# Optimization experiments

Hardware: AMD Instinct MI355X
Metric: run time of the kernel (lower is better)

## Reference

```python
import jax, jax.numpy as jnp
import numpy as np

B, IN, HID, GH, K, A = 131072, 256, 128, 64, 4, 3
EPS = 1e-5

def _ln(x, g, b):
    mu = jnp.mean(x, axis=-1, keepdims=True)
    var = jnp.mean((x - mu) ** 2, axis=-1, keepdims=True)
    return (x - mu) * jax.lax.rsqrt(var + EPS) * g + b

def _expert(x, blend, W, bias):
    # math-equivalent to einsum('bk,koi->boi') + bmm: blend after per-expert matvec
    per_exp = jnp.einsum('bi,koi->bko', x, W)          # [B,K,out]
    return jnp.einsum('bk,bko->bo', blend, per_exp) + blend @ bias

def setup_inputs() -> dict:
    key = jax.random.key(0)
    ks = jax.random.split(key, 8)
    d = {}
    d['state'] = jax.random.normal(ks[0], (B, IN), jnp.float32)
    # gating network
    d['gw1'] = jax.random.normal(ks[1], (GH, IN), jnp.float32) / np.sqrt(IN)
    d['gb1'] = jnp.zeros((GH,), jnp.float32)
    d['gln_g'] = jnp.ones((GH,), jnp.float32)
    d['gln_b'] = jnp.zeros((GH,), jnp.float32)
    d['gw2'] = jax.random.normal(ks[2], (K, GH), jnp.float32) / np.sqrt(GH)
    d['gb2'] = jnp.zeros((K,), jnp.float32)
    d['temperature'] = jnp.ones((1,), jnp.float32)
    # experts: weight [K, out, in] with kaiming-like init sqrt(2/in)
    d['e1_w'] = jax.random.normal(ks[3], (K, HID, IN), jnp.float32) * np.sqrt(2.0 / IN)
    d['e1_b'] = jnp.zeros((K, HID), jnp.float32)
    d['ln1_g'] = jnp.ones((HID,), jnp.float32)
    d['ln1_b'] = jnp.zeros((HID,), jnp.float32)
    d['e2_w'] = jax.random.normal(ks[4], (K, HID, HID), jnp.float32) * np.sqrt(2.0 / HID)
    d['e2_b'] = jnp.zeros((K, HID), jnp.float32)
    d['ln2_g'] = jnp.ones((HID,), jnp.float32)
    d['ln2_b'] = jnp.zeros((HID,), jnp.float32)
    d['e3_w'] = jax.random.normal(ks[5], (K, A, HID), jnp.float32) * np.sqrt(2.0 / HID)
    d['e3_b'] = jnp.zeros((K, A), jnp.float32)
    return d

def reference(state, gw1, gb1, gln_g, gln_b, gw2, gb2, temperature,
              e1_w, e1_b, ln1_g, ln1_b, e2_w, e2_b, ln2_g, ln2_b, e3_w, e3_b):
    # gating
    h = jax.nn.relu(_ln(state @ gw1.T + gb1, gln_g, gln_b))
    logits = h @ gw2.T + gb2
    temp = jnp.clip(temperature, 0.1, 2.0)
    blend = jax.nn.softmax(logits / temp, axis=-1)       # [B,K]
    # expert stack
    x = jax.nn.relu(_ln(_expert(state, blend, e1_w, e1_b), ln1_g, ln1_b))
    x = jax.nn.relu(_ln(_expert(x, blend, e2_w, e2_b), ln2_g, ln2_b))
    policy_logits = _expert(x, blend, e3_w, e3_b)        # [B,A]
    return policy_logits, blend
```

## Files before the change

kernel.cpp:

```cpp
#include <hip/hip_runtime.h>


typedef __attribute__((ext_vector_type(8))) short short8;
typedef __attribute__((ext_vector_type(4))) float f32x4;

constexpr int B_TOT = 131072;
constexpr int IN    = 256;
constexpr int HID   = 128;
constexpr int GH    = 64;
constexpr int NA    = 3;
constexpr int ROWS  = 64;
constexpr int XS    = 264;
constexpr int BS    = 132;
constexpr float EPS = 1e-5f;

constexpr int O_G1H = 0;
constexpr int O_E1H = 32768;
constexpr int O_E2H = 294912;

__device__ __forceinline__ unsigned short bf16h(float f) {
  unsigned int u = __float_as_uint(f);
  return (unsigned short)((u + 0x7FFFu + ((u >> 16) & 1u)) >> 16);
}
__device__ __forceinline__ float bf16f(unsigned short h) {
  return __uint_as_float(((unsigned int)h) << 16);
}

__global__ __launch_bounds__(256) void prep_w(
    const float* __restrict__ gw1, const float* __restrict__ e1w,
    const float* __restrict__ e2w, unsigned short* __restrict__ ws)
{
  const int NT = 16384 + 131072 + 65536;
  for (int d = blockIdx.x * 256 + threadIdx.x; d < NT; d += gridDim.x * 256) {
    float v; int dst, lo_off;
    if (d < 16384) {
      int d2 = d; int j = d2 & 7, lane = (d2 >> 3) & 63, kc = (d2 >> 9) & 7, gt = d2 >> 12;
      int o = gt * 16 + (lane & 15), k = kc * 32 + (lane >> 4) * 8 + j;
      v = gw1[o * IN + k]; dst = O_G1H + d2; lo_off = 16384;
    } else if (d < 147456) {
      int d2 = d - 16384; int j = d2 & 7, lane = (d2 >> 3) & 63, kc = (d2 >> 9) & 7,
          ot = (d2 >> 12) & 7, ke = d2 >> 15;
      int o = ot * 16 + (lane & 15), k = kc * 32 + (lane >> 4) * 8 + j;
      v = e1w[ke * HID * IN + o * IN + k]; dst = O_E1H + d2; lo_off = 131072;
    } else {
      int d2 = d - 147456; int j = d2 & 7, lane = (d2 >> 3) & 63, kc = (d2 >> 9) & 3,
          ot = (d2 >> 11) & 7, ke = d2 >> 14;
      int o = ot * 16 + (lane & 15), k = kc * 32 + (lane >> 4) * 8 + j;
      v = e2w[ke * HID * HID + o * HID + k]; dst = O_E2H + d2; lo_off = 65536;
    }
    unsigned short h = bf16h(v);
    ws[dst] = h;
    ws[dst + lo_off] = bf16h(v - bf16f(h));
  }
}

#define MFMA(a, b, c) __builtin_amdgcn_mfma_f32_16x16x32_bf16((a), (b), (c), 0, 0, 0)

__global__ __launch_bounds__(512) void mann_mfma(
    const float* __restrict__ state,
    const float* __restrict__ gb1,
    const float* __restrict__ gln_g, const float* __restrict__ gln_b,
    const float* __restrict__ gw2, const float* __restrict__ gb2,
    const float* __restrict__ temperature,
    const float* __restrict__ e1_b,
    const float* __restrict__ ln1_g, const float* __restrict__ ln1_b,
    const float* __restrict__ e2_b,
    const float* __restrict__ ln2_g, const float* __restrict__ ln2_b,
    const float* __restrict__ e3_w, const float* __restrict__ e3_b,
    const unsigned short* __restrict__ wf,
    float* __restrict__ out_policy, float* __restrict__ out_blend)
{
  __shared__ __align__(16) unsigned char smem[75264];
  unsigned short* xh = (unsigned short*)smem;
  unsigned short* xl = (unsigned short*)(smem + 33792);
  unsigned short* ah = (unsigned short*)smem;
  unsigned short* al = (unsigned short*)(smem + 16384);
  float* bt    = (float*)(smem + 33792);
  float* ps    = (float*)(smem + 67584);
  float* stats = (float*)(smem + 69632);
  float* lp    = (float*)(smem + 70144);
  float* sbl   = (float*)(smem + 74240);

  const int tid = threadIdx.x;
  const int lane = tid & 63, wv = tid >> 6;
  const int l15 = lane & 15, l4 = lane >> 4;
  const int rh = wv >> 2, oq = wv & 3;
  const int rowbase = blockIdx.x * ROWS;
  const f32x4 zz = {0.f, 0.f, 0.f, 0.f};

  {
    const float4* gsrc = (const float4*)(state + (size_t)rowbase * IN);
#pragma unroll
    for (int it = 0; it < 8; ++it) {
      int fi = tid + it * 512;
      int row = fi >> 6, c4 = fi & 63;
      float4 v = gsrc[fi];
      int base = row * XS + c4 * 4;
      float vv[4] = {v.x, v.y, v.z, v.w};
#pragma unroll
      for (int e = 0; e < 4; ++e) {
        unsigned short h = bf16h(vv[e]);
        xh[base + e] = h;
        xl[base + e] = bf16h(vv[e] - bf16f(h));
      }
    }
  }
  __syncthreads();

  {
    f32x4 g[2] = {zz, zz};
    const unsigned short* wpg = wf + O_G1H + (oq * 8 * 64 + (size_t)lane) * 8;
#pragma unroll 1
    for (int kc = 0; kc < 8; ++kc) {
      short8 wh = *(const short8*)(wpg + kc * 512);
      short8 wl = *(const short8*)(wpg + kc * 512 + 16384);
#pragma unroll
      for (int rt = 0; rt < 2; ++rt) {
        int row = rh * 32 + rt * 16 + l15;
        int xo = row * XS + kc * 32 + l4 * 8;
        short8 xhf = *(const short8*)&xh[xo];
        short8 xlf = *(const short8*)&xl[xo];
        g[rt] = MFMA(xhf, wh, g[rt]);
        g[rt] = MFMA(xlf, wh, g[rt]);
        g[rt] = MFMA(xhf, wl, g[rt]);
      }
    }
    const float bv = gb1[oq * 16 + l15];
#pragma unroll
    for (int rt = 0; rt < 2; ++rt)
#pragma unroll
      for (int r = 0; r < 4; ++r) {
        g[rt][r] += bv;
        float sv = g[rt][r], qv = g[rt][r] * g[rt][r];
#pragma unroll
        for (int m = 1; m < 16; m <<= 1) { sv += __shfl_xor(sv, m, 64); qv += __shfl_xor(qv, m, 64); }
        if (l15 == 0) {
          int row = rh * 32 + rt * 16 + l4 * 4 + r;
          ps[(row * 4 + oq) * 2 + 0] = sv;
          ps[(row * 4 + oq) * 2 + 1] = qv;
        }
      }
    __syncthreads();
    if (tid < 64) {
      float s = 0.f, q = 0.f;
#pragma unroll
      for (int o = 0; o < 4; ++o) { s += ps[(tid * 4 + o) * 2]; q += ps[(tid * 4 + o) * 2 + 1]; }
      float mu = s * (1.f / GH), var = q * (1.f / GH) - mu * mu;
      stats[tid * 2] = mu; stats[tid * 2 + 1] = rsqrtf(var + EPS);
    }
    __syncthreads();
    const float gg = gln_g[oq * 16 + l15], gbb = gln_b[oq * 16 + l15];
    float g2[4];
#pragma unroll
    for (int k = 0; k < 4; ++k) g2[k] = gw2[k * GH + oq * 16 + l15];
#pragma unroll
    for (int rt = 0; rt < 2; ++rt)
#pragma unroll
      for (int r = 0; r < 4; ++r) {
        int row = rh * 32 + rt * 16 + l4 * 4 + r;
        float mu = stats[row * 2], rstd = stats[row * 2 + 1];
        float h = fmaxf((g[rt][r] - mu) * rstd * gg + gbb, 0.f);
#pragma unroll
        for (int k = 0; k < 4; ++k) {
          float pv = h * g2[k];
#pragma unroll
          for (int m = 1; m < 16; m <<= 1) pv += __shfl_xor(pv, m, 64);
          if (l15 == 0) lp[(row * 4 + oq) * 4 + k] = pv;
        }
      }
  }
  __syncthreads();

  if (tid < 256) {
    int row = tid >> 2, kk = tid & 3;
    float lg = lp[(row * 4 + 0) * 4 + kk] + lp[(row * 4 + 1) * 4 + kk] +
               lp[(row * 4 + 2) * 4 + kk] + lp[(row * 4 + 3) * 4 + kk] + gb2[kk];
    float t = fminf(fmaxf(temperature[0], 0.1f), 2.0f);
    lg /= t;
    float mx = lg;
    mx = fmaxf(mx, __shfl_xor(mx, 1, 64));
    mx = fmaxf(mx, __shfl_xor(mx, 2, 64));
    float e = expf(lg - mx);
    float su = e;
    su += __shfl_xor(su, 1, 64);
    su += __shfl_xor(su, 2, 64);
    float bl = e / su;
    sbl[row * 4 + kk] = bl;
    out_blend[(size_t)(rowbase + row) * 4 + kk] = bl;
  }
  __syncthreads();

  f32x4 accb[2][2] = {{zz, zz}, {zz, zz}};

#pragma unroll
  for (int ke = 0; ke < 4; ++ke) {
    f32x4 t[2][2] = {{zz, zz}, {zz, zz}};
    const unsigned short* wp1 = wf + O_E1H + (((ke * 8 + oq * 2) * 8) * 64 + (size_t)lane) * 8;
#pragma unroll 1
    for (int kc = 0; kc < 8; ++kc) {
      short8 xhf[2], xlf[2];
#pragma unroll
      for (int rt = 0; rt < 2; ++rt) {
        int row = rh * 32 + rt * 16 + l15;
        int xo = row * XS + kc * 32 + l4 * 8;
        xhf[rt] = *(const short8*)&xh[xo];
        xlf[rt] = *(const short8*)&xl[xo];
      }
#pragma unroll
      for (int ot = 0; ot < 2; ++ot) {
        const unsigned short* p = wp1 + ot * 4096 + kc * 512;
        short8 wh = *(const short8*)p;
        short8 wl = *(const short8*)(p + 131072);
#pragma unroll
        for (int rt = 0; rt < 2; ++rt) {
          t[rt][ot] = MFMA(xhf[rt], wh, t[rt][ot]);
          t[rt][ot] = MFMA(xlf[rt], wh, t[rt][ot]);
          t[rt][ot] = MFMA(xhf[rt], wl, t[rt][ot]);
        }
      }
    }
    const float bv0 = e1_b[ke * HID + oq * 32 + l15];
    const float bv1 = e1_b[ke * HID + oq * 32 + 16 + l15];
#pragma unroll
    for (int rt = 0; rt < 2; ++rt)
#pragma unroll
      for (int r = 0; r < 4; ++r) {
        int row = rh * 32 + rt * 16 + l4 * 4 + r;
        float blv = sbl[row * 4 + ke];
        accb[rt][0][r] += blv * (t[rt][0][r] + bv0);
        accb[rt][1][r] += blv * (t[rt][1][r] + bv1);
      }
  }
#pragma unroll
  for (int rt = 0; rt < 2; ++rt)
#pragma unroll
    for (int r = 0; r < 4; ++r) {
      float sv = accb[rt][0][r] + accb[rt][1][r];
      float qv = accb[rt][0][r] * accb[rt][0][r] + accb[rt][1][r] * accb[rt][1][r];
#pragma unroll
      for (int m = 1; m < 16; m <<= 1) { sv += __shfl_xor(sv, m, 64); qv += __shfl_xor(qv, m, 64); }
      if (l15 == 0) {
        int row = rh * 32 + rt * 16 + l4 * 4 + r;
        ps[(row * 4 + oq) * 2 + 0] = sv;
        ps[(row * 4 + oq) * 2 + 1] = qv;
      }
    }
  __syncthreads();
  if (tid < 64) {
    float s = 0.f, q = 0.f;
#pragma unroll
    for (int o = 0; o < 4; ++o) { s += ps[(tid * 4 + o) * 2]; q += ps[(tid * 4 + o) * 2 + 1]; }
    float mu = s * (1.f / HID), var = q * (1.f / HID) - mu * mu;
    stats[tid * 2] = mu; stats[tid * 2 + 1] = rsqrtf(var + EPS);
  }
  __syncthreads();
  {
#pragma unroll
    for (int ot = 0; ot < 2; ++ot) {
      int c = oq * 32 + ot * 16 + l15;
      float lgv = ln1_g[c], lbv = ln1_b[c];
#pragma unroll
      for (int rt = 0; rt < 2; ++rt)
#pragma unroll
        for (int r = 0; r < 4; ++r) {
          int row = rh * 32 + rt * 16 + l4 * 4 + r;
          float mu = stats[row * 2], rstd = stats[row * 2 + 1];
          float y = fmaxf((accb[rt][ot][r] - mu) * rstd * lgv + lbv, 0.f);
          unsigned short h = bf16h(y);
          int idx = row * HID + (((c >> 3) ^ (row & 7)) << 3) + (c & 7);
          ah[idx] = h; al[idx] = bf16h(y - bf16f(h));
        }
    }
  }
  __syncthreads();

#pragma unroll
  for (int rt = 0; rt < 2; ++rt)
#pragma unroll
    for (int ot = 0; ot < 2; ++ot) accb[rt][ot] = zz;
#pragma unroll
  for (int ke = 0; ke < 4; ++ke) {
    f32x4 t[2][2] = {{zz, zz}, {zz, zz}};
    const unsigned short* wp2 = wf + O_E2H + (((ke * 8 + oq * 2) * 4) * 64 + (size_t)lane) * 8;
#pragma unroll 1
    for (int kc = 0; kc < 4; ++kc) {
      short8 xhf[2], xlf[2];
#pragma unroll
      for (int rt = 0; rt < 2; ++rt) {
        int row = rh * 32 + rt * 16 + l15;
        int gidx = (kc * 4 + l4) ^ (row & 7);
        int idx = row * HID + gidx * 8;
        xhf[rt] = *(const short8*)&ah[idx];
        xlf[rt] = *(const short8*)&al[idx];
      }
#pragma unroll
      for (int ot = 0; ot < 2; ++ot) {
        const unsigned short* p = wp2 + ot * 2048 + kc * 512;
        short8 wh = *(const short8*)p;
        short8 wl = *(const short8*)(p + 65536);
#pragma unroll
        for (int rt = 0; rt < 2; ++rt) {
          t[rt][ot] = MFMA(xhf[rt], wh, t[rt][ot]);
          t[rt][ot] = MFMA(xlf[rt], wh, t[rt][ot]);
          t[rt][ot] = MFMA(xhf[rt], wl, t[rt][ot]);
        }
      }
    }
    const float bv0 = e2_b[ke * HID + oq * 32 + l15];
    const float bv1 = e2_b[ke * HID + oq * 32 + 16 + l15];
#pragma unroll
    for (int rt = 0; rt < 2; ++rt)
#pragma unroll
      for (int r = 0; r < 4; ++r) {
        int row = rh * 32 + rt * 16 + l4 * 4 + r;
        float blv = sbl[row * 4 + ke];
        accb[rt][0][r] += blv * (t[rt][0][r] + bv0);
        accb[rt][1][r] += blv * (t[rt][1][r] + bv1);
      }
  }
#pragma unroll
  for (int rt = 0; rt < 2; ++rt)
#pragma unroll
    for (int r = 0; r < 4; ++r) {
      float sv = accb[rt][0][r] + accb[rt][1][r];
      float qv = accb[rt][0][r] * accb[rt][0][r] + accb[rt][1][r] * accb[rt][1][r];
#pragma unroll
      for (int m = 1; m < 16; m <<= 1) { sv += __shfl_xor(sv, m, 64); qv += __shfl_xor(qv, m, 64); }
      if (l15 == 0) {
        int row = rh * 32 + rt * 16 + l4 * 4 + r;
        ps[(row * 4 + oq) * 2 + 0] = sv;
        ps[(row * 4 + oq) * 2 + 1] = qv;
      }
    }
  __syncthreads();
  if (tid < 64) {
    float s = 0.f, q = 0.f;
#pragma unroll
    for (int o = 0; o < 4; ++o) { s += ps[(tid * 4 + o) * 2]; q += ps[(tid * 4 + o) * 2 + 1]; }
    float mu = s * (1.f / HID), var = q * (1.f / HID) - mu * mu;
    stats[tid * 2] = mu; stats[tid * 2 + 1] = rsqrtf(var + EPS);
  }
  __syncthreads();
  {
#pragma unroll
    for (int ot = 0; ot < 2; ++ot) {
      int c = oq * 32 + ot * 16 + l15;
      float lgv = ln2_g[c], lbv = ln2_b[c];
#pragma unroll
      for (int rt = 0; rt < 2; ++rt)
#pragma unroll
        for (int r = 0; r < 4; ++r) {
          int row = rh * 32 + rt * 16 + l4 * 4 + r;
          float mu = stats[row * 2], rstd = stats[row * 2 + 1];
          float y = fmaxf((accb[rt][ot][r] - mu) * rstd * lgv + lbv, 0.f);
          bt[row * BS + c] = y;
        }
    }
  }
  __syncthreads();

  if (tid < 256) {
    int row = tid >> 2, kk = tid & 3;
    float p[NA] = {0.f, 0.f, 0.f};
#pragma unroll
    for (int ic = 0; ic < HID / 4; ++ic) {
      float4 xv = *(const float4*)&bt[row * BS + ic * 4];
#pragma unroll
      for (int a = 0; a < NA; ++a) {
        float4 wv = *(const float4*)&e3_w[(size_t)(kk * NA + a) * HID + ic * 4];
        p[a] = fmaf(xv.x, wv.x, fmaf(xv.y, wv.y, fmaf(xv.z, wv.z, fmaf(xv.w, wv.w, p[a]))));
      }
    }
    float blk = sbl[row * 4 + kk];
#pragma unroll
    for (int a = 0; a < NA; ++a) p[a] = blk * (p[a] + e3_b[kk * NA + a]);
#pragma unroll
    for (int a = 0; a < NA; ++a) {
      p[a] += __shfl_xor(p[a], 1, 64);
      p[a] += __shfl_xor(p[a], 2, 64);
    }
    if (kk == 0) {
      size_t o = (size_t)(rowbase + row) * NA;
      out_policy[o + 0] = p[0];
      out_policy[o + 1] = p[1];
      out_policy[o + 2] = p[2];
    }
  }
}

extern "C" void kernel_launch(void* const* d_in, const int* in_sizes, int n_in,
                              void* d_out, int out_size, void* d_ws, size_t ws_size,
                              hipStream_t stream) {
  const float* state = (const float*)d_in[0];
  const float* gw1   = (const float*)d_in[1];
  const float* gb1   = (const float*)d_in[2];
  const float* gln_g = (const float*)d_in[3];
  const float* gln_b = (const float*)d_in[4];
  const float* gw2   = (const float*)d_in[5];
  const float* gb2   = (const float*)d_in[6];
  const float* temp  = (const float*)d_in[7];
  const float* e1_w  = (const float*)d_in[8];
  const float* e1_b  = (const float*)d_in[9];
  const float* ln1_g = (const float*)d_in[10];
  const float* ln1_b = (const float*)d_in[11];
  const float* e2_w  = (const float*)d_in[12];
  const float* e2_b  = (const float*)d_in[13];
  const float* ln2_g = (const float*)d_in[14];
  const float* ln2_b = (const float*)d_in[15];
  const float* e3_w  = (const float*)d_in[16];
  const float* e3_b  = (const float*)d_in[17];

  unsigned short* wf = (unsigned short*)d_ws;
  float* out_policy = (float*)d_out;
  float* out_blend  = (float*)d_out + (size_t)B_TOT * NA;

  prep_w<<<832, 256, 0, stream>>>(gw1, e1_w, e2_w, wf);
  mann_mfma<<<B_TOT / ROWS, 512, 0, stream>>>(
      state, gb1, gln_g, gln_b, gw2, gb2, temp,
      e1_b, ln1_g, ln1_b, e2_b, ln2_g, ln2_b, e3_w, e3_b,
      wf, out_policy, out_blend);
}
```

Before: 600.4 us.

## Shrink row tile to 48, remap waves to output columns, swizzle LDS, atomic LN stats

Reduces the rows per block from 64 to 48 and gives each of the 8 waves a 16-column output slice over all 48 rows, where before waves were split by row half and column quarter. The padded LDS layouts are replaced with XOR-swizzled layouts, and the per-row LayerNorm partial sums are combined with LDS atomics instead of a partial-sum buffer. Together these cut shared memory to about 50KB and add a launch bound that asks for more resident waves, to improve occupancy and latency hiding. In exchange each wave reloads the activation tile for three row tiles, the grid gets a ragged tail with bounds checks, and the atomics change the floating-point summation order.

```diff
diff --git a/kernel.cpp b/kernel.cpp
--- a/kernel.cpp
+++ b/kernel.cpp
@@ -7,16 +7,9 @@
 constexpr int B_TOT = 131072;
 constexpr int IN    = 256;
 constexpr int HID   = 128;
-constexpr int GH    = 64;
 constexpr int NA    = 3;
-constexpr int ROWS  = 64;
-constexpr int XS    = 264;
-constexpr int BS    = 132;
+constexpr int ROWS  = 48;
 constexpr float EPS = 1e-5f;
-
-constexpr int O_G1H = 0;
-constexpr int O_E1H = 32768;
-constexpr int O_E2H = 294912;
 
 __device__ __forceinline__ unsigned short bf16h(float f) {
   unsigned int u = __float_as_uint(f);
@@ -36,17 +29,17 @@
     if (d < 16384) {
       int d2 = d; int j = d2 & 7, lane = (d2 >> 3) & 63, kc = (d2 >> 9) & 7, gt = d2 >> 12;
       int o = gt * 16 + (lane & 15), k = kc * 32 + (lane >> 4) * 8 + j;
-      v = gw1[o * IN + k]; dst = O_G1H + d2; lo_off = 16384;
+      v = gw1[o * IN + k]; dst = d2; lo_off = 16384;
     } else if (d < 147456) {
       int d2 = d - 16384; int j = d2 & 7, lane = (d2 >> 3) & 63, kc = (d2 >> 9) & 7,
           ot = (d2 >> 12) & 7, ke = d2 >> 15;
       int o = ot * 16 + (lane & 15), k = kc * 32 + (lane >> 4) * 8 + j;
-      v = e1w[ke * HID * IN + o * IN + k]; dst = O_E1H + d2; lo_off = 131072;
+      v = e1w[ke * HID * IN + o * IN + k]; dst = 32768 + d2; lo_off = 131072;
     } else {
       int d2 = d - 147456; int j = d2 & 7, lane = (d2 >> 3) & 63, kc = (d2 >> 9) & 3,
           ot = (d2 >> 11) & 7, ke = d2 >> 14;
       int o = ot * 16 + (lane & 15), k = kc * 32 + (lane >> 4) * 8 + j;
-      v = e2w[ke * HID * HID + o * HID + k]; dst = O_E2H + d2; lo_off = 65536;
+      v = e2w[ke * HID * HID + o * HID + k]; dst = 294912 + d2; lo_off = 65536;
     }
     unsigned short h = bf16h(v);
     ws[dst] = h;
@@ -56,7 +49,7 @@
 
 #define MFMA(a, b, c) __builtin_amdgcn_mfma_f32_16x16x32_bf16((a), (b), (c), 0, 0, 0)
 
-__global__ __launch_bounds__(512) void mann_mfma(
+__global__ __launch_bounds__(512, 6) void mann_mfma(
     const float* __restrict__ state,
     const float* __restrict__ gb1,
     const float* __restrict__ gln_g, const float* __restrict__ gln_b,
@@ -70,32 +63,32 @@
     const unsigned short* __restrict__ wf,
     float* __restrict__ out_policy, float* __restrict__ out_blend)
 {
-  __shared__ __align__(16) unsigned char smem[75264];
+  __shared__ __align__(16) unsigned char smem[50304];
   unsigned short* xh = (unsigned short*)smem;
-  unsigned short* xl = (unsigned short*)(smem + 33792);
+  unsigned short* xl = (unsigned short*)(smem + 24576);
   unsigned short* ah = (unsigned short*)smem;
-  unsigned short* al = (unsigned short*)(smem + 16384);
-  float* bt    = (float*)(smem + 33792);
-  float* ps    = (float*)(smem + 67584);
-  float* stats = (float*)(smem + 69632);
-  float* lp    = (float*)(smem + 70144);
-  float* sbl   = (float*)(smem + 74240);
-
-  const int tid = threadIdx.x;
+  unsigned short* al = (unsigned short*)(smem + 12288);
+  float* bt    = (float*)(smem + 24576);
+  float* stats = (float*)(smem + 49152);
+  float* sbl   = (float*)(smem + 49536);
+
+  const int tid  = threadIdx.x;
   const int lane = tid & 63, wv = tid >> 6;
-  const int l15 = lane & 15, l4 = lane >> 4;
-  const int rh = wv >> 2, oq = wv & 3;
+  const int l15  = lane & 15, l4 = lane >> 4;
   const int rowbase = blockIdx.x * ROWS;
+  const int valid = (B_TOT - rowbase) < ROWS ? (B_TOT - rowbase) : ROWS;
   const f32x4 zz = {0.f, 0.f, 0.f, 0.f};
 
   {
-    const float4* gsrc = (const float4*)(state + (size_t)rowbase * IN);
-#pragma unroll
-    for (int it = 0; it < 8; ++it) {
+    const float4* gsrc = reinterpret_cast<const float4*>(state) + (size_t)rowbase * 64;
+#pragma unroll
+    for (int it = 0; it < 6; ++it) {
       int fi = tid + it * 512;
       int row = fi >> 6, c4 = fi & 63;
-      float4 v = gsrc[fi];
-      int base = row * XS + c4 * 4;
+      float4 v = {0.f, 0.f, 0.f, 0.f};
+      if (row < valid) v = gsrc[fi];
+      int g = c4 >> 1;
+      int base = row * 256 + ((g ^ (row & 7)) << 3) + (c4 & 1) * 4;
       float vv[4] = {v.x, v.y, v.z, v.w};
 #pragma unroll
       for (int e = 0; e < 4; ++e) {
@@ -104,30 +97,31 @@
         xl[base + e] = bf16h(vv[e] - bf16f(h));
       }
     }
-  }
-  __syncthreads();
-
-  {
-    f32x4 g[2] = {zz, zz};
-    const unsigned short* wpg = wf + O_G1H + (oq * 8 * 64 + (size_t)lane) * 8;
+    if (tid < 288) ((float*)(smem + 49152))[tid] = 0.f;
+  }
+  __syncthreads();
+
+  f32x4 g[3] = {zz, zz, zz};
+  if (wv < 4) {
+    const unsigned short* wpg = wf + (size_t)wv * 4096 + lane * 8;
 #pragma unroll 1
     for (int kc = 0; kc < 8; ++kc) {
       short8 wh = *(const short8*)(wpg + kc * 512);
       short8 wl = *(const short8*)(wpg + kc * 512 + 16384);
 #pragma unroll
-      for (int rt = 0; rt < 2; ++rt) {
-        int row = rh * 32 + rt * 16 + l15;
-        int xo = row * XS + kc * 32 + l4 * 8;
-        short8 xhf = *(const short8*)&xh[xo];
-        short8 xlf = *(const short8*)&xl[xo];
+      for (int rt = 0; rt < 3; ++rt) {
+        int row = rt * 16 + l15;
+        int idx = row * 256 + (((kc * 4 + l4) ^ (row & 7)) << 3);
+        short8 xhf = *(const short8*)&xh[idx];
+        short8 xlf = *(const short8*)&xl[idx];
         g[rt] = MFMA(xhf, wh, g[rt]);
         g[rt] = MFMA(xlf, wh, g[rt]);
         g[rt] = MFMA(xhf, wl, g[rt]);
       }
     }
-    const float bv = gb1[oq * 16 + l15];
-#pragma unroll
-    for (int rt = 0; rt < 2; ++rt)
+    const float bv = gb1[wv * 16 + l15];
+#pragma unroll
+    for (int rt = 0; rt < 3; ++rt)
 #pragma unroll
       for (int r = 0; r < 4; ++r) {
         g[rt][r] += bv;
@@ -135,29 +129,29 @@
 #pragma unroll
         for (int m = 1; m < 16; m <<= 1) { sv += __shfl_xor(sv, m, 64); qv += __shfl_xor(qv, m, 64); }
         if (l15 == 0) {
-          int row = rh * 32 + rt * 16 + l4 * 4 + r;
-          ps[(row * 4 + oq) * 2 + 0] = sv;
-          ps[(row * 4 + oq) * 2 + 1] = qv;
+          int row = rt * 16 + l4 * 4 + r;
+          atomicAdd(&stats[row * 2 + 0], sv);
+          atomicAdd(&stats[row * 2 + 1], qv);
         }
       }
-    __syncthreads();
-    if (tid < 64) {
-      float s = 0.f, q = 0.f;
-#pragma unroll
-      for (int o = 0; o < 4; ++o) { s += ps[(tid * 4 + o) * 2]; q += ps[(tid * 4 + o) * 2 + 1]; }
-      float mu = s * (1.f / GH), var = q * (1.f / GH) - mu * mu;
-      stats[tid * 2] = mu; stats[tid * 2 + 1] = rsqrtf(var + EPS);
-    }
-    __syncthreads();
-    const float gg = gln_g[oq * 16 + l15], gbb = gln_b[oq * 16 + l15];
+  }
+  __syncthreads();
+  if (tid < ROWS) {
+    float s = stats[tid * 2], q = stats[tid * 2 + 1];
+    float mu = s * (1.f / 64.f), var = q * (1.f / 64.f) - mu * mu;
+    stats[tid * 2] = mu; stats[tid * 2 + 1] = rsqrtf(var + EPS);
+  }
+  __syncthreads();
+  if (wv < 4) {
+    const float gg = gln_g[wv * 16 + l15], gbb = gln_b[wv * 16 + l15];
     float g2[4];
 #pragma unroll
-    for (int k = 0; k < 4; ++k) g2[k] = gw2[k * GH + oq * 16 + l15];
-#pragma unroll
-    for (int rt = 0; rt < 2; ++rt)
-#pragma unroll
-      for (int r = 0; r < 4; ++r) {
-        int row = rh * 32 + rt * 16 + l4 * 4 + r;
+    for (int k = 0; k < 4; ++k) g2[k] = gw2[k * 64 + wv * 16 + l15];
+#pragma unroll
+    for (int rt = 0; rt < 3; ++rt)
+#pragma unroll
+      for (int r = 0; r < 4; ++r) {
+        int row = rt * 16 + l4 * 4 + r;
         float mu = stats[row * 2], rstd = stats[row * 2 + 1];
         float h = fmaxf((g[rt][r] - mu) * rstd * gg + gbb, 0.f);
 #pragma unroll
@@ -165,18 +159,16 @@
           float pv = h * g2[k];
 #pragma unroll
           for (int m = 1; m < 16; m <<= 1) pv += __shfl_xor(pv, m, 64);
-          if (l15 == 0) lp[(row * 4 + oq) * 4 + k] = pv;
+          if (l15 == 0) atomicAdd(&sbl[row * 4 + k], pv);
         }
       }
   }
   __syncthreads();
-
-  if (tid < 256) {
-    int row = tid >> 2, kk = tid & 3;
-    float lg = lp[(row * 4 + 0) * 4 + kk] + lp[(row * 4 + 1) * 4 + kk] +
-               lp[(row * 4 + 2) * 4 + kk] + lp[(row * 4 + 3) * 4 + kk] + gb2[kk];
-    float t = fminf(fmaxf(temperature[0], 0.1f), 2.0f);
-    lg /= t;
+  if (tid < ROWS * 4) {
+    int row = tid >> 2, k = tid & 3;
+    float lg = sbl[tid] + gb2[k];
+    float tt = fminf(fmaxf(temperature[0], 0.1f), 2.0f);
+    lg /= tt;
     float mx = lg;
     mx = fmaxf(mx, __shfl_xor(mx, 1, 64));
     mx = fmaxf(mx, __shfl_xor(mx, 2, 64));
@@ -185,205 +177,176 @@
     su += __shfl_xor(su, 1, 64);
     su += __shfl_xor(su, 2, 64);
     float bl = e / su;
-    sbl[row * 4 + kk] = bl;
-    out_blend[(size_t)(rowbase + row) * 4 + kk] = bl;
-  }
-  __syncthreads();
-
-  f32x4 accb[2][2] = {{zz, zz}, {zz, zz}};
-
-#pragma unroll
+    sbl[tid] = bl;
+    if (row < valid) out_blend[(size_t)(rowbase + row) * 4 + k] = bl;
+  } else if (tid < 288) {
+    stats[tid - 192] = 0.f;
+  }
+  __syncthreads();
+
+  f32x4 accb[3] = {zz, zz, zz};
+#pragma unroll 1
   for (int ke = 0; ke < 4; ++ke) {
-    f32x4 t[2][2] = {{zz, zz}, {zz, zz}};
-    const unsigned short* wp1 = wf + O_E1H + (((ke * 8 + oq * 2) * 8) * 64 + (size_t)lane) * 8;
+    f32x4 t[3] = {zz, zz, zz};
+    const unsigned short* wp = wf + 32768 + (size_t)(ke * 8 + wv) * 4096 + lane * 8;
 #pragma unroll 1
     for (int kc = 0; kc < 8; ++kc) {
-      short8 xhf[2], xlf[2];
-#pragma unroll
-      for (int rt = 0; rt < 2; ++rt) {
-        int row = rh * 32 + rt * 16 + l15;
-        int xo = row * XS + kc * 32 + l4 * 8;
-        xhf[rt] = *(const short8*)&xh[xo];
-        xlf[rt] = *(const short8*)&xl[xo];
-      }
-#pragma unroll
-      for (int ot = 0; ot < 2; ++ot) {
-        const unsigned short* p = wp1 + ot * 4096 + kc * 512;
-        short8 wh = *(const short8*)p;
-        short8 wl = *(const short8*)(p + 131072);
-#pragma unroll
-        for (int rt = 0; rt < 2; ++rt) {
-          t[rt][ot] = MFMA(xhf[rt], wh, t[rt][ot]);
-          t[rt][ot] = MFMA(xlf[rt], wh, t[rt][ot]);
-          t[rt][ot] = MFMA(xhf[rt], wl, t[rt][ot]);
-        }
-      }
-    }
-    const float bv0 = e1_b[ke * HID + oq * 32 + l15];
-    const float bv1 = e1_b[ke * HID + oq * 32 + 16 + l15];
-#pragma unroll
-    for (int rt = 0; rt < 2; ++rt)
-#pragma unroll
-      for (int r = 0; r < 4; ++r) {
-        int row = rh * 32 + rt * 16 + l4 * 4 + r;
+      short8 wh = *(const short8*)(wp + kc * 512);
+      short8 wl = *(const short8*)(wp + kc * 512 + 131072);
+#pragma unroll
+      for (int rt = 0; rt < 3; ++rt) {
+        int row = rt * 16 + l15;
+        int idx = row * 256 + (((kc * 4 + l4) ^ (row & 7)) << 3);
+        short8 xhf = *(const short8*)&xh[idx];
+        short8 xlf = *(const short8*)&xl[idx];
+        t[rt] = MFMA(xhf, wh, t[rt]);
+        t[rt] = MFMA(xlf, wh, t[rt]);
+        t[rt] = MFMA(xhf, wl, t[rt]);
+      }
+    }
+    const float bv = e1_b[ke * HID + wv * 16 + l15];
+#pragma unroll
+    for (int rt = 0; rt < 3; ++rt)
+#pragma unroll
+      for (int r = 0; r < 4; ++r) {
+        int row = rt * 16 + l4 * 4 + r;
         float blv = sbl[row * 4 + ke];
-        accb[rt][0][r] += blv * (t[rt][0][r] + bv0);
-        accb[rt][1][r] += blv * (t[rt][1][r] + bv1);
-      }
-  }
-#pragma unroll
-  for (int rt = 0; rt < 2; ++rt)
+        accb[rt][r] += blv * (t[rt][r] + bv);
+      }
+  }
+#pragma unroll
+  for (int rt = 0; rt < 3; ++rt)
 #pragma unroll
     for (int r = 0; r < 4; ++r) {
-      float sv = accb[rt][0][r] + accb[rt][1][r];
-      float qv = accb[rt][0][r] * accb[rt][0][r] + accb[rt][1][r] * accb[rt][1][r];
+      float sv = accb[rt][r], qv = accb[rt][r] * accb[rt][r];
 #pragma unroll
       for (int m = 1; m < 16; m <<= 1) { sv += __shfl_xor(sv, m, 64); qv += __shfl_xor(qv, m, 64); }
       if (l15 == 0) {
-        int row = rh * 32 + rt * 16 + l4 * 4 + r;
-        ps[(row * 4 + oq) * 2 + 0] = sv;
-        ps[(row * 4 + oq) * 2 + 1] = qv;
-      }
-    }
-  __syncthreads();
-  if (tid < 64) {
-    float s = 0.f, q = 0.f;
-#pragma unroll
-    for (int o = 0; o < 4; ++o) { s += ps[(tid * 4 + o) * 2]; q += ps[(tid * 4 + o) * 2 + 1]; }
-    float mu = s * (1.f / HID), var = q * (1.f / HID) - mu * mu;
+        int row = rt * 16 + l4 * 4 + r;
+        atomicAdd(&stats[row * 2 + 0], sv);
+        atomicAdd(&stats[row * 2 + 1], qv);
+      }
+    }
+  __syncthreads();
+  if (tid < ROWS) {
+    float s = stats[tid * 2], q = stats[tid * 2 + 1];
+    float mu = s * (1.f / 128.f), var = q * (1.f / 128.f) - mu * mu;
     stats[tid * 2] = mu; stats[tid * 2 + 1] = rsqrtf(var + EPS);
   }
   __syncthreads();
   {
-#pragma unroll
-    for (int ot = 0; ot < 2; ++ot) {
-      int c = oq * 32 + ot * 16 + l15;
-      float lgv = ln1_g[c], lbv = ln1_b[c];
-#pragma unroll
-      for (int rt = 0; rt < 2; ++rt)
-#pragma unroll
-        for (int r = 0; r < 4; ++r) {
-          int row = rh * 32 + rt * 16 + l4 * 4 + r;
-          float mu = stats[row * 2], rstd = stats[row * 2 + 1];
-          float y = fmaxf((accb[rt][ot][r] - mu) * rstd * lgv + lbv, 0.f);
-          unsigned short h = bf16h(y);
-          int idx = row * HID + (((c >> 3) ^ (row & 7)) << 3) + (c & 7);
-          ah[idx] = h; al[idx] = bf16h(y - bf16f(h));
-        }
-    }
-  }
-  __syncthreads();
-
-#pragma unroll
-  for (int rt = 0; rt < 2; ++rt)
-#pragma unroll
-    for (int ot = 0; ot < 2; ++ot) accb[rt][ot] = zz;
-#pragma unroll
+    const float lgv = ln1_g[wv * 16 + l15], lbv = ln1_b[wv * 16 + l15];
+#pragma unroll
+    for (int rt = 0; rt < 3; ++rt)
+#pragma unroll
+      for (int r = 0; r < 4; ++r) {
+        int row = rt * 16 + l4 * 4 + r;
+        float mu = stats[row * 2], rstd = stats[row * 2 + 1];
+        float y = fmaxf((accb[rt][r] - mu) * rstd * lgv + lbv, 0.f);
+        unsigned short h = bf16h(y);
+        int g16 = (wv * 2 + (l15 >> 3)) ^ (row & 7);
+        int idx = row * 128 + g16 * 8 + (l15 & 7);
+        ah[idx] = h; al[idx] = bf16h(y - bf16f(h));
+      }
+  }
+  __syncthreads();
+  if (tid < 96) stats[tid] = 0.f;
+  __syncthreads();
+
+  accb[0] = zz; accb[1] = zz; accb[2] = zz;
+#pragma unroll 1
   for (int ke = 0; ke < 4; ++ke) {
-    f32x4 t[2][2] = {{zz, zz}, {zz, zz}};
-    const unsigned short* wp2 = wf + O_E2H + (((ke * 8 + oq * 2) * 4) * 64 + (size_t)lane) * 8;
+    f32x4 t[3] = {zz, zz, zz};
+    const unsigned short* wp = wf + 294912 + (size_t)(ke * 8 + wv) * 2048 + lane * 8;
 #pragma unroll 1
     for (int kc = 0; kc < 4; ++kc) {
-      short8 xhf[2], xlf[2];
-#pragma unroll
-      for (int rt = 0; rt < 2; ++rt) {
-        int row = rh * 32 + rt * 16 + l15;
-        int gidx = (kc * 4 + l4) ^ (row & 7);
-        int idx = row * HID + gidx * 8;
-        xhf[rt] = *(const short8*)&ah[idx];
-        xlf[rt] = *(const short8*)&al[idx];
-      }
-#pragma unroll
-      for (int ot = 0; ot < 2; ++ot) {
-        const unsigned short* p = wp2 + ot * 2048 + kc * 512;
-        short8 wh = *(const short8*)p;
-        short8 wl = *(const short8*)(p + 65536);
-#pragma unroll
-        for (int rt = 0; rt < 2; ++rt) {
-          t[rt][ot] = MFMA(xhf[rt], wh, t[rt][ot]);
-          t[rt][ot] = MFMA(xlf[rt], wh, t[rt][ot]);
-          t[rt][ot] = MFMA(xhf[rt], wl, t[rt][ot]);
-        }
-      }
-    }
-    const float bv0 = e2_b[ke * HID + oq * 32 + l15];
-    const float bv1 = e2_b[ke * HID + oq * 32 + 16 + l15];
-#pragma unroll
-    for (int rt = 0; rt < 2; ++rt)
-#pragma unroll
-      for (int r = 0; r < 4; ++r) {
-        int row = rh * 32 + rt * 16 + l4 * 4 + r;
+      short8 wh = *(const short8*)(wp + kc * 512);
+      short8 wl = *(const short8*)(wp + kc * 512 + 65536);
+#pragma unroll
+      for (int rt = 0; rt < 3; ++rt) {
+        int row = rt * 16 + l15;
+        int gi = (kc * 4 + l4) ^ (row & 7);
+        int idx = row * 128 + gi * 8;
+        short8 xhf = *(const short8*)&ah[idx];
+        short8 xlf = *(const short8*)&al[idx];
+        t[rt] = MFMA(xhf, wh, t[rt]);
+        t[rt] = MFMA(xlf, wh, t[rt]);
+        t[rt] = MFMA(xhf, wl, t[rt]);
+      }
+    }
+    const float bv = e2_b[ke * HID + wv * 16 + l15];
+#pragma unroll
+    for (int rt = 0; rt < 3; ++rt)
+#pragma unroll
+      for (int r = 0; r < 4; ++r) {
+        int row = rt * 16 + l4 * 4 + r;
         float blv = sbl[row * 4 + ke];
-        accb[rt][0][r] += blv * (t[rt][0][r] + bv0);
-        accb[rt][1][r] += blv * (t[rt][1][r] + bv1);
-      }
-  }
-#pragma unroll
-  for (int rt = 0; rt < 2; ++rt)
+        accb[rt][r] += blv * (t[rt][r] + bv);
+      }
+  }
+#pragma unroll
+  for (int rt = 0; rt < 3; ++rt)
 #pragma unroll
     for (int r = 0; r < 4; ++r) {
-      float sv = accb[rt][0][r] + accb[rt][1][r];
-      float qv = accb[rt][0][r] * accb[rt][0][r] + accb[rt][1][r] * accb[rt][1][r];
+      float sv = accb[rt][r], qv = accb[rt][r] * accb[rt][r];
 #pragma unroll
       for (int m = 1; m < 16; m <<= 1) { sv += __shfl_xor(sv, m, 64); qv += __shfl_xor(qv, m, 64); }
       if (l15 == 0) {
-        int row = rh * 32 + rt * 16 + l4 * 4 + r;
-        ps[(row * 4 + oq) * 2 + 0] = sv;
-        ps[(row * 4 + oq) * 2 + 1] = qv;
-      }
-    }
-  __syncthreads();
-  if (tid < 64) {
-    float s = 0.f, q = 0.f;
-#pragma unroll
-    for (int o = 0; o < 4; ++o) { s += ps[(tid * 4 + o) * 2]; q += ps[(tid * 4 + o) * 2 + 1]; }
-    float mu = s * (1.f / HID), var = q * (1.f / HID) - mu * mu;
+        int row = rt * 16 + l4 * 4 + r;
+        atomicAdd(&stats[row * 2 + 0], sv);
+        atomicAdd(&stats[row * 2 + 1], qv);
+      }
+    }
+  __syncthreads();
+  if (tid < ROWS) {
+    float s = stats[tid * 2], q = stats[tid * 2 + 1];
+    float mu = s * (1.f / 128.f), var = q * (1.f / 128.f) - mu * mu;
     stats[tid * 2] = mu; stats[tid * 2 + 1] = rsqrtf(var + EPS);
   }
   __syncthreads();
   {
-#pragma unroll
-    for (int ot = 0; ot < 2; ++ot) {
-      int c = oq * 32 + ot * 16 + l15;
-      float lgv = ln2_g[c], lbv = ln2_b[c];
-#pragma unroll
-      for (int rt = 0; rt < 2; ++rt)
-#pragma unroll
-        for (int r = 0; r < 4; ++r) {
-          int row = rh * 32 + rt * 16 + l4 * 4 + r;
-          float mu = stats[row * 2], rstd = stats[row * 2 + 1];
-          float y = fmaxf((accb[rt][ot][r] - mu) * rstd * lgv + lbv, 0.f);
-          bt[row * BS + c] = y;
-        }
-    }
-  }
-  __syncthreads();
-
-  if (tid < 256) {
+    const float lgv = ln2_g[wv * 16 + l15], lbv = ln2_b[wv * 16 + l15];
+#pragma unroll
+    for (int rt = 0; rt < 3; ++rt)
+#pragma unroll
+      for (int r = 0; r < 4; ++r) {
+        int row = rt * 16 + l4 * 4 + r;
+        float mu = stats[row * 2], rstd = stats[row * 2 + 1];
+        float y = fmaxf((accb[rt][r] - mu) * rstd * lgv + lbv, 0.f);
+        int c = wv * 16 + l15;
+        int gf = (wv * 4 + (l15 >> 2)) ^ (row & 7);
+        bt[row * 128 + gf * 4 + (c & 3)] = y;
+      }
+  }
+  __syncthreads();
+
+  if (tid < ROWS * 4) {
     int row = tid >> 2, kk = tid & 3;
-    float p[NA] = {0.f, 0.f, 0.f};
-#pragma unroll
-    for (int ic = 0; ic < HID / 4; ++ic) {
-      float4 xv = *(const float4*)&bt[row * BS + ic * 4];
-#pragma unroll
-      for (int a = 0; a < NA; ++a) {
-        float4 wv = *(const float4*)&e3_w[(size_t)(kk * NA + a) * HID + ic * 4];
-        p[a] = fmaf(xv.x, wv.x, fmaf(xv.y, wv.y, fmaf(xv.z, wv.z, fmaf(xv.w, wv.w, p[a]))));
-      }
+    float p0 = 0.f, p1 = 0.f, p2 = 0.f;
+    const float* w3 = e3_w + (size_t)kk * NA * HID;
+#pragma unroll 1
+    for (int ic = 0; ic < 32; ++ic) {
+      int gi = ic ^ (row & 7);
+      float4 xv = *(const float4*)&bt[row * 128 + gi * 4];
+      float4 w0 = *(const float4*)&w3[0 * HID + ic * 4];
+      float4 w1 = *(const float4*)&w3[1 * HID + ic * 4];
+      float4 w2 = *(const float4*)&w3[2 * HID + ic * 4];
+      p0 = fmaf(xv.x, w0.x, fmaf(xv.y, w0.y, fmaf(xv.z, w0.z, fmaf(xv.w, w0.w, p0))));
+      p1 = fmaf(xv.x, w1.x, fmaf(xv.y, w1.y, fmaf(xv.z, w1.z, fmaf(xv.w, w1.w, p1))));
+      p2 = fmaf(xv.x, w2.x, fmaf(xv.y, w2.y, fmaf(xv.z, w2.z, fmaf(xv.w, w2.w, p2))));
     }
     float blk = sbl[row * 4 + kk];
-#pragma unroll
-    for (int a = 0; a < NA; ++a) p[a] = blk * (p[a] + e3_b[kk * NA + a]);
-#pragma unroll
-    for (int a = 0; a < NA; ++a) {
-      p[a] += __shfl_xor(p[a], 1, 64);
-      p[a] += __shfl_xor(p[a], 2, 64);
-    }
-    if (kk == 0) {
+    p0 = blk * (p0 + e3_b[kk * NA + 0]);
+    p1 = blk * (p1 + e3_b[kk * NA + 1]);
+    p2 = blk * (p2 + e3_b[kk * NA + 2]);
+    p0 += __shfl_xor(p0, 1, 64); p0 += __shfl_xor(p0, 2, 64);
+    p1 += __shfl_xor(p1, 1, 64); p1 += __shfl_xor(p1, 2, 64);
+    p2 += __shfl_xor(p2, 1, 64); p2 += __shfl_xor(p2, 2, 64);
+    if (kk == 0 && row < valid) {
       size_t o = (size_t)(rowbase + row) * NA;
-      out_policy[o + 0] = p[0];
-      out_policy[o + 1] = p[1];
-      out_policy[o + 2] = p[2];
+      out_policy[o + 0] = p0;
+      out_policy[o + 1] = p1;
+      out_policy[o + 2] = p2;
     }
   }
 }
@@ -415,7 +378,8 @@
   float* out_blend  = (float*)d_out + (size_t)B_TOT * NA;
 
   prep_w<<<832, 256, 0, stream>>>(gw1, e1_w, e2_w, wf);
-  mann_mfma<<<B_TOT / ROWS, 512, 0, stream>>>(
+  const int grid = (B_TOT + ROWS - 1) / ROWS;
+  mann_mfma<<<grid, 512, 0, stream>>>(
       state, gb1, gln_g, gln_b, gw2, gb2, temp,
       e1_b, ln1_g, ln1_b, e2_b, ln2_g, ln2_b, e3_w, e3_b,
       wf, out_policy, out_blend);
```

New measurement: 481.1 us. 19.9% less time.
